# Performance work log

Hardware: AMD Instinct MI355X
Metric: run time of the kernel (lower is better)

The kernel has to match this reference:

```python
import jax, jax.numpy as jnp
import numpy as np

SCOPE = 2
N = 20
D = 64
CAP = 32
IN_CH = 64
OUT_CH = 64
FIN_CH = 64
WIDTH = 2 * SCOPE + 1


def setup_inputs() -> dict:
    key = jax.random.key(0)
    ks = jax.random.split(key, 7)
    dm = 3 * CAP + D  # memory feature dim: 3 relpos blocks + spatial embedding

    def w(k, fan_in, shape):
        return jax.random.normal(k, shape, jnp.float32) / np.sqrt(fan_in)

    return dict(
        spatial_embeddings=jax.random.normal(ks[0], (N, N, N, D), jnp.float32),
        relpos_w=jax.random.normal(ks[1], (WIDTH, CAP), jnp.float32) / np.sqrt(WIDTH * CAP),
        Wq=w(ks[2], D, (D, IN_CH)), bq=jnp.zeros((IN_CH,), jnp.float32),
        Wk=w(ks[3], dm, (dm, IN_CH)), bk=jnp.zeros((IN_CH,), jnp.float32),
        Wv=w(ks[4], dm, (dm, OUT_CH)), bv=jnp.zeros((OUT_CH,), jnp.float32),
        Wo=w(ks[5], OUT_CH, (OUT_CH, FIN_CH)), bo=jnp.zeros((FIN_CH,), jnp.float32),
    )


def reference(spatial_embeddings, relpos_w, Wq, bq, Wk, bk, Wv, bv, Wo, bo):
    n = spatial_embeddings.shape[0]
    w = WIDTH
    m = n + 2 * SCOPE  # padded grid size
    cap = relpos_w.shape[-1]

    # within_edges=False: zero-pad all three spatial axes by SCOPE
    se = jnp.pad(spatial_embeddings, ((SCOPE, SCOPE),) * 3 + ((0, 0),))
    central = SCOPE + jnp.arange(n)               # padded centre indices [n]
    off = jnp.arange(-SCOPE, SCOPE + 1)           # [w]
    idx = central[:, None] + off[None, :]         # [n, w] padded neighbour indices

    # relative-position cube: relpos_cube[x,y,z] = concat(r[x], r[y], r[z])
    r0 = jnp.broadcast_to(relpos_w[:, None, None, :], (w, w, w, cap))
    r1 = jnp.broadcast_to(relpos_w[None, :, None, :], (w, w, w, cap))
    r2 = jnp.broadcast_to(relpos_w[None, None, :, :], (w, w, w, cap))
    relpos_flat = jnp.concatenate([r0, r1, r2], axis=-1).reshape(w * w * w, 3 * cap)

    # neighbour gather replicating jnp.meshgrid(...)'s default 'xy' indexing:
    # cube[b, a, c] = se[ni[a], nj[b], nk[c]]
    ii = idx[:, None, None, None, :, None]        # (qi, a)
    jj = idx[None, :, None, :, None, None]        # (qj, b)
    kk = idx[None, None, :, None, None, :]        # (qk, c)
    nb = se[ii, jj, kk]                           # [n,n,n,w,w,w,D]
    nb = nb.reshape(n, n, n, w * w * w, -1)       # [n,n,n,w^3,D]

    # keys/values over memory = concat(relpos, neighbours); split the weight
    Wk_rel, Wk_nb = Wk[:3 * cap], Wk[3 * cap:]
    Wv_rel, Wv_nb = Wv[:3 * cap], Wv[3 * cap:]
    k_rel = relpos_flat @ Wk_rel + bk             # [w^3, IN_CH] (query-independent)
    v_rel = relpos_flat @ Wv_rel + bv             # [w^3, OUT_CH]
    keys = k_rel + jnp.einsum('xyzpd,dc->xyzpc', nb, Wk_nb)
    values = v_rel + jnp.einsum('xyzpd,dc->xyzpc', nb, Wv_nb)

    # centre embedding at padded index `central` == original unpadded embedding
    q = spatial_embeddings @ Wq + bq              # [n,n,n,IN_CH]
    logits = jnp.einsum('xyzc,xyzpc->xyzp', q, keys)

    # edge mask, built in (a,b,c) cube order (faithful to original's flatten order)
    valid = ((idx > SCOPE) & (idx < m - SCOPE)).astype(logits.dtype)  # [n, w]
    mask = (valid[:, None, None, :, None, None]
            * valid[None, :, None, None, :, None]
            * valid[None, None, :, None, None, :]).reshape(n, n, n, w * w * w)
    logits = logits - (1.0 - mask) * 1e9

    scores = jax.nn.softmax(logits, axis=-1)
    reweighted = jnp.einsum('xyzp,xyzpc->xyzc', scores, values)
    return reweighted @ Wo + bo                   # [n,n,n,FIN_CH]
```

## Files before the change

kernel.cpp:

```cpp
#include <hip/hip_runtime.h>

#define NN 20
#define NP 125
#define NV (NN*NN*NN)

__global__ __launch_bounds__(64) void prep(
        const float* __restrict__ rpw,
        const float* __restrict__ Wk, const float* __restrict__ bk,
        const float* __restrict__ Wv, const float* __restrict__ bv,
        const float* __restrict__ Wo,
        float* __restrict__ k_rel, float* __restrict__ vrelW,
        float* __restrict__ Wvo) {
    const int c = threadIdx.x;
    if (blockIdx.x < NP) {
        const int p = blockIdx.x;
        const int d3 = p / 25, d4 = (p / 5) % 5, d5 = p % 5;
        __shared__ float vtmp[64];
        float ak = bk[c], av = bv[c];
#pragma unroll
        for (int t = 0; t < 96; ++t) {
            const int blk = t >> 5, off = t & 31;
            const int row = (blk == 0) ? d3 : (blk == 1) ? d4 : d5;
            const float r = rpw[row * 32 + off];
            ak = fmaf(r, Wk[t * 64 + c], ak);
            av = fmaf(r, Wv[t * 64 + c], av);
        }
        k_rel[p * 64 + c] = ak;
        vtmp[c] = av;
        __syncthreads();
        float o = 0.f;
#pragma unroll 8
        for (int e = 0; e < 64; ++e)
            o = fmaf(vtmp[e], Wo[e * 64 + c], o);
        vrelW[p * 64 + c] = o;
    } else {
        const int d = blockIdx.x - NP;
        float acc = 0.f;
#pragma unroll 8
        for (int e = 0; e < 64; ++e)
            acc = fmaf(Wv[(96 + d) * 64 + e], Wo[e * 64 + c], acc);
        Wvo[d * 64 + c] = acc;
    }
}

__global__ __launch_bounds__(256) void qkv2(
        const float* __restrict__ SE,
        const float* __restrict__ Wq, const float* __restrict__ bq,
        const float* __restrict__ Wk, const float* __restrict__ Wvo,
        float* __restrict__ Q, float* __restrict__ Km, float* __restrict__ VW) {
    __shared__ float se_s[32][65];
    const int t = threadIdx.x;
    const int vbase = blockIdx.x * 32;
    {
        const float4* __restrict__ src = (const float4*)(SE + vbase * 64);
        const float4 a = src[t];
        const float4 b = src[t + 256];
        const int r0 = t >> 4,        c0 = (t & 15) * 4;
        const int r1 = (t + 256) >> 4;
        se_s[r0][c0 + 0] = a.x; se_s[r0][c0 + 1] = a.y;
        se_s[r0][c0 + 2] = a.z; se_s[r0][c0 + 3] = a.w;
        se_s[r1][c0 + 0] = b.x; se_s[r1][c0 + 1] = b.y;
        se_s[r1][c0 + 2] = b.z; se_s[r1][c0 + 3] = b.w;
    }
    __syncthreads();
    const int lane = t & 63, w = t >> 6;
    float aq[8], ak[8], av[8];
#pragma unroll
    for (int j = 0; j < 8; ++j) { aq[j] = bq[lane]; ak[j] = 0.f; av[j] = 0.f; }
#pragma unroll 8
    for (int d = 0; d < 64; ++d) {
        const float wq = Wq[d * 64 + lane];
        const float wk = Wk[(96 + d) * 64 + lane];
        const float wv = Wvo[d * 64 + lane];
#pragma unroll
        for (int j = 0; j < 8; ++j) {
            const float s = se_s[w * 8 + j][d];
            aq[j] = fmaf(s, wq, aq[j]);
            ak[j] = fmaf(s, wk, ak[j]);
            av[j] = fmaf(s, wv, av[j]);
        }
    }
#pragma unroll
    for (int j = 0; j < 8; ++j) {
        const int v = vbase + w * 8 + j;
        Q[v * 64 + lane]  = aq[j];
        Km[v * 64 + lane] = ak[j];
        VW[v * 64 + lane] = av[j];
    }
}

__global__ __launch_bounds__(512, 4) void attn4(
        const float* __restrict__ Q, const float* __restrict__ Km,
        const float* __restrict__ VW,
        const float* __restrict__ k_rel, const float* __restrict__ vrelW,
        const float* __restrict__ bo,
        float* __restrict__ out) {
    __shared__ float u[216 * 65];
    __shared__ float sc_s[8][128];

    const int tid  = threadIdx.x;
    const int lane = tid & 63;
    const int w    = tid >> 6;

    const int chunk = blockIdx.x & 7;
    const int idx   = blockIdx.x >> 3;
    const int cx = chunk >> 2, cy = (chunk >> 1) & 1, cz = chunk & 1;
    const int TX = cx * 5 + idx / 25;
    const int TY = cy * 5 + (idx / 5) % 5;
    const int TZ = cz * 5 + idx % 5;

    const int wx = w >> 2, wy = (w >> 1) & 1, wz = w & 1;
    const int x = TX * 2 + wx, y = TY * 2 + wy, z = TZ * 2 + wz;
    const int v = (x * NN + y) * NN + z;

    for (int i = tid; i < 216 * 16; i += 512) {
        const int row = i >> 4, ch = i & 15;
        const int ux = row / 36, uy = (row / 6) % 6, uz = row % 6;
        const int gX = TX * 2 - 2 + ux;
        const int gY = TY * 2 - 2 + uy;
        const int gZ = TZ * 2 - 2 + uz;
        float4 val = make_float4(0.f, 0.f, 0.f, 0.f);
        if ((unsigned)gX <= 19u && (unsigned)gY <= 19u && (unsigned)gZ <= 19u)
            val = ((const float4*)Km)[((gX * NN + gY) * NN + gZ) * 16 + ch];
        const int b = row * 65 + ch * 4;
        u[b] = val.x; u[b + 1] = val.y; u[b + 2] = val.z; u[b + 3] = val.w;
    }

    const float q = Q[v * 64 + lane];
    const int p0 = lane;
    const int p1 = lane + 64;
    const int p1c = (p1 < NP) ? p1 : (NP - 1);

    int e3 = p0 / 25, e4 = (p0 / 5) % 5, e5 = p0 % 5;
    const int row0 = 36 * (wx + e4) + 6 * (wy + e3) + (wz + e5);
    const bool mv0 = ((unsigned)(x + e3 - 3) <= 18u) &&
                     ((unsigned)(y + e4 - 3) <= 18u) &&
                     ((unsigned)(z + e5 - 3) <= 18u);
    e3 = p1c / 25; e4 = (p1c / 5) % 5; e5 = p1c % 5;
    const int row1 = 36 * (wx + e4) + 6 * (wy + e3) + (wz + e5);
    const bool mv1 = (p1 < NP) &&
                     ((unsigned)(x + e3 - 3) <= 18u) &&
                     ((unsigned)(y + e4 - 3) <= 18u) &&
                     ((unsigned)(z + e5 - 3) <= 18u);

    const float4* __restrict__ kr0 = (const float4*)(k_rel + p0 * 64);
    const float4* __restrict__ kr1 = (const float4*)(k_rel + p1c * 64);

    __syncthreads();

    float a0 = 0.f, a1 = 0.f;
#pragma unroll
    for (int i = 0; i < 16; ++i) {
        const float qa = __shfl(q, 4 * i + 0);
        const float qb = __shfl(q, 4 * i + 1);
        const float qc = __shfl(q, 4 * i + 2);
        const float qd = __shfl(q, 4 * i + 3);
        const float4 r0 = kr0[i], r1 = kr1[i];
        const int b0 = row0 * 65 + 4 * i;
        const int b1 = row1 * 65 + 4 * i;
        a0 = fmaf(u[b0] + r0.x, qa, a0);
        a0 = fmaf(u[b0 + 1] + r0.y, qb, a0);
        a0 = fmaf(u[b0 + 2] + r0.z, qc, a0);
        a0 = fmaf(u[b0 + 3] + r0.w, qd, a0);
        a1 = fmaf(u[b1] + r1.x, qa, a1);
        a1 = fmaf(u[b1 + 1] + r1.y, qb, a1);
        a1 = fmaf(u[b1 + 2] + r1.z, qc, a1);
        a1 = fmaf(u[b1 + 3] + r1.w, qd, a1);
    }
    const float l0 = mv0 ? a0 : -1e9f;
    const float l1 = mv1 ? a1 : -1e9f;

    float m = fmaxf(l0, l1);
#pragma unroll
    for (int d = 1; d < 64; d <<= 1) m = fmaxf(m, __shfl_xor(m, d));
    const float e0 = __expf(l0 - m);
    const float e1 = __expf(l1 - m);
    float ssum = e0 + e1;
#pragma unroll
    for (int d = 1; d < 64; d <<= 1) ssum += __shfl_xor(ssum, d);
    const float inv = 1.f / ssum;
    sc_s[w][p0] = e0 * inv;
    sc_s[w][p1] = e1 * inv;
    __syncthreads();

    for (int i = tid; i < 216 * 16; i += 512) {
        const int row = i >> 4, ch = i & 15;
        const int ux = row / 36, uy = (row / 6) % 6, uz = row % 6;
        const int gX = TX * 2 - 2 + ux;
        const int gY = TY * 2 - 2 + uy;
        const int gZ = TZ * 2 - 2 + uz;
        float4 val = make_float4(0.f, 0.f, 0.f, 0.f);
        if ((unsigned)gX <= 19u && (unsigned)gY <= 19u && (unsigned)gZ <= 19u)
            val = ((const float4*)VW)[((gX * NN + gY) * NN + gZ) * 16 + ch];
        const int b = row * 65 + ch * 4;
        u[b] = val.x; u[b + 1] = val.y; u[b + 2] = val.z; u[b + 3] = val.w;
    }
    __syncthreads();

    float A0 = 0.f, A1 = 0.f, A2 = 0.f, A3 = 0.f, A4 = 0.f;
    const float* __restrict__ vr = vrelW + lane;
#pragma unroll 5
    for (int g = 0; g < 25; ++g) {
        const int ge3 = g / 5, ge4 = g % 5;
        const int rb = 36 * (wx + ge4) + 6 * (wy + ge3) + wz;
        const int pb = g * 5;
        A0 = fmaf(sc_s[w][pb + 0], u[(rb + 0) * 65 + lane] + vr[(pb + 0) * 64], A0);
        A1 = fmaf(sc_s[w][pb + 1], u[(rb + 1) * 65 + lane] + vr[(pb + 1) * 64], A1);
        A2 = fmaf(sc_s[w][pb + 2], u[(rb + 2) * 65 + lane] + vr[(pb + 2) * 64], A2);
        A3 = fmaf(sc_s[w][pb + 3], u[(rb + 3) * 65 + lane] + vr[(pb + 3) * 64], A3);
        A4 = fmaf(sc_s[w][pb + 4], u[(rb + 4) * 65 + lane] + vr[(pb + 4) * 64], A4);
    }
    const float rw = ((A0 + A1) + (A2 + A3)) + A4;
    out[v * 64 + lane] = rw + bo[lane];
}

extern "C" void kernel_launch(void* const* d_in, const int* in_sizes, int n_in,
                              void* d_out, int out_size, void* d_ws, size_t ws_size,
                              hipStream_t stream) {
    const float* SE  = (const float*)d_in[0];
    const float* rpw = (const float*)d_in[1];
    const float* Wq  = (const float*)d_in[2];
    const float* bq  = (const float*)d_in[3];
    const float* Wk  = (const float*)d_in[4];
    const float* bk  = (const float*)d_in[5];
    const float* Wv  = (const float*)d_in[6];
    const float* bv  = (const float*)d_in[7];
    const float* Wo  = (const float*)d_in[8];
    const float* bo  = (const float*)d_in[9];
    float* out = (float*)d_out;

    float* ws    = (float*)d_ws;
    float* Q     = ws;
    float* Km    = ws + 512000;
    float* VW    = ws + 1024000;
    float* k_rel = ws + 1536000;
    float* vrelW = ws + 1544000;
    float* Wvo   = ws + 1552000;

    prep<<<NP + 64, 64, 0, stream>>>(rpw, Wk, bk, Wv, bv, Wo, k_rel, vrelW, Wvo);
    qkv2<<<NV / 32, 256, 0, stream>>>(SE, Wq, bq, Wk, Wvo, Q, Km, VW);
    attn4<<<1000, 512, 0, stream>>>(Q, Km, VW, k_rel, vrelW, bo, out);
}
```

Before: 134.9 us.

## Precompute q·k_rel in projection kernel, swizzle LDS, prefetch values into registers

The query-times-relative-key dot products are moved out of the attention kernel: the projection kernel now computes q·k_rel for all 125 offsets per voxel and writes them to a new workspace buffer. The attention kernel reads these and no longer adds k_rel inside its inner loop. Shared memory switches from a 65-float padded stride to a 68-float stride with XOR swizzle, so float4 LDS reads are possible. The VW halo is loaded into registers before the logits loop, overlapping global latency with compute, and shuffles become readlane. In exchange the projection kernel does more work, adds 4 MB of extra traffic and uses more registers.

```diff
diff --git a/kernel.cpp b/kernel.cpp
--- a/kernel.cpp
+++ b/kernel.cpp
@@ -3,6 +3,10 @@
 #define NN 20
 #define NP 125
 #define NV (NN*NN*NN)
+
+__device__ __forceinline__ float rlf(float v, int l) {
+    return __uint_as_float(__builtin_amdgcn_readlane(__float_as_uint(v), l));
+}
 
 __global__ __launch_bounds__(64) void prep(
         const float* __restrict__ rpw,
@@ -43,12 +47,15 @@
     }
 }
 
-__global__ __launch_bounds__(256) void qkv2(
+__global__ __launch_bounds__(256) void qkv4(
         const float* __restrict__ SE,
         const float* __restrict__ Wq, const float* __restrict__ bq,
         const float* __restrict__ Wk, const float* __restrict__ Wvo,
-        float* __restrict__ Q, float* __restrict__ Km, float* __restrict__ VW) {
+        const float* __restrict__ k_rel,
+        float* __restrict__ Q, float* __restrict__ Km, float* __restrict__ VW,
+        float* __restrict__ qkr) {
     __shared__ float se_s[32][65];
+    __shared__ __align__(16) float krs[125 * 68];
     const int t = threadIdx.x;
     const int vbase = blockIdx.x * 32;
     {
@@ -62,6 +69,12 @@
         se_s[r1][c0 + 0] = b.x; se_s[r1][c0 + 1] = b.y;
         se_s[r1][c0 + 2] = b.z; se_s[r1][c0 + 3] = b.w;
     }
+    for (int i = t; i < 125 * 16; i += 256) {
+        const int row = i >> 4, ch4 = (i & 15) * 4;
+        const float4 val = ((const float4*)k_rel)[row * 16 + (ch4 >> 2)];
+        const int xk = ((row >> 3) & 7) << 2;
+        *(float4*)&krs[row * 68 + (ch4 ^ xk)] = val;
+    }
     __syncthreads();
     const int lane = t & 63, w = t >> 6;
     float aq[8], ak[8], av[8];
@@ -87,15 +100,40 @@
         Km[v * 64 + lane] = ak[j];
         VW[v * 64 + lane] = av[j];
     }
-}
-
-__global__ __launch_bounds__(512, 4) void attn4(
+    const int p0 = lane;
+    const int p1c = (lane + 64 < NP) ? (lane + 64) : (NP - 1);
+    const int xk0 = ((p0 >> 3) & 7) << 2;
+    const int xk1 = ((p1c >> 3) & 7) << 2;
+#pragma unroll
+    for (int j = 0; j < 8; ++j) {
+        float d0 = 0.f, d1 = 0.f;
+#pragma unroll
+        for (int i = 0; i < 16; ++i) {
+            const float qa = rlf(aq[j], 4 * i + 0);
+            const float qb = rlf(aq[j], 4 * i + 1);
+            const float qc = rlf(aq[j], 4 * i + 2);
+            const float qd = rlf(aq[j], 4 * i + 3);
+            const float4 k0 = *(const float4*)&krs[p0 * 68 + ((4 * i) ^ xk0)];
+            const float4 k1 = *(const float4*)&krs[p1c * 68 + ((4 * i) ^ xk1)];
+            d0 = fmaf(k0.x, qa, d0); d0 = fmaf(k0.y, qb, d0);
+            d0 = fmaf(k0.z, qc, d0); d0 = fmaf(k0.w, qd, d0);
+            d1 = fmaf(k1.x, qa, d1); d1 = fmaf(k1.y, qb, d1);
+            d1 = fmaf(k1.z, qc, d1); d1 = fmaf(k1.w, qd, d1);
+        }
+        const int v = vbase + w * 8 + j;
+        qkr[v * 128 + lane] = d0;
+        qkr[v * 128 + 64 + lane] = d1;
+    }
+}
+
+#define XU(row) ((((row >> 3) ^ (row >> 6)) & 7) << 2)
+
+__global__ __launch_bounds__(512, 4) void attn9(
         const float* __restrict__ Q, const float* __restrict__ Km,
-        const float* __restrict__ VW,
-        const float* __restrict__ k_rel, const float* __restrict__ vrelW,
-        const float* __restrict__ bo,
+        const float* __restrict__ VW, const float* __restrict__ qkr,
+        const float* __restrict__ vrelW, const float* __restrict__ bo,
         float* __restrict__ out) {
-    __shared__ float u[216 * 65];
+    __shared__ __align__(16) float u[216 * 68];
     __shared__ float sc_s[8][128];
 
     const int tid  = threadIdx.x;
@@ -114,19 +152,21 @@
     const int v = (x * NN + y) * NN + z;
 
     for (int i = tid; i < 216 * 16; i += 512) {
-        const int row = i >> 4, ch = i & 15;
+        const int row = i >> 4, ch4 = (i & 15) * 4;
         const int ux = row / 36, uy = (row / 6) % 6, uz = row % 6;
         const int gX = TX * 2 - 2 + ux;
         const int gY = TY * 2 - 2 + uy;
         const int gZ = TZ * 2 - 2 + uz;
         float4 val = make_float4(0.f, 0.f, 0.f, 0.f);
         if ((unsigned)gX <= 19u && (unsigned)gY <= 19u && (unsigned)gZ <= 19u)
-            val = ((const float4*)Km)[((gX * NN + gY) * NN + gZ) * 16 + ch];
-        const int b = row * 65 + ch * 4;
-        u[b] = val.x; u[b + 1] = val.y; u[b + 2] = val.z; u[b + 3] = val.w;
+            val = ((const float4*)Km)[((gX * NN + gY) * NN + gZ) * 16 + (ch4 >> 2)];
+        *(float4*)&u[row * 68 + (ch4 ^ XU(row))] = val;
     }
 
     const float q = Q[v * 64 + lane];
+    const float qk0 = qkr[v * 128 + lane];
+    const float qk1 = qkr[v * 128 + 64 + lane];
+
     const int p0 = lane;
     const int p1 = lane + 64;
     const int p1c = (p1 < NP) ? p1 : (NP - 1);
@@ -142,33 +182,43 @@
                      ((unsigned)(x + e3 - 3) <= 18u) &&
                      ((unsigned)(y + e4 - 3) <= 18u) &&
                      ((unsigned)(z + e5 - 3) <= 18u);
-
-    const float4* __restrict__ kr0 = (const float4*)(k_rel + p0 * 64);
-    const float4* __restrict__ kr1 = (const float4*)(k_rel + p1c * 64);
-
-    __syncthreads();
+    const int xu0 = XU(row0), xu1 = XU(row1);
+
+    __syncthreads();
+
+    float4 vwreg[7];
+#pragma unroll
+    for (int k = 0; k < 7; ++k) {
+        const int i = tid + 512 * k;
+        float4 val = make_float4(0.f, 0.f, 0.f, 0.f);
+        if (i < 216 * 16) {
+            const int row = i >> 4, ch = i & 15;
+            const int ux = row / 36, uy = (row / 6) % 6, uz = row % 6;
+            const int gX = TX * 2 - 2 + ux;
+            const int gY = TY * 2 - 2 + uy;
+            const int gZ = TZ * 2 - 2 + uz;
+            if ((unsigned)gX <= 19u && (unsigned)gY <= 19u && (unsigned)gZ <= 19u)
+                val = ((const float4*)VW)[((gX * NN + gY) * NN + gZ) * 16 + ch];
+        }
+        vwreg[k] = val;
+    }
 
     float a0 = 0.f, a1 = 0.f;
 #pragma unroll
     for (int i = 0; i < 16; ++i) {
-        const float qa = __shfl(q, 4 * i + 0);
-        const float qb = __shfl(q, 4 * i + 1);
-        const float qc = __shfl(q, 4 * i + 2);
-        const float qd = __shfl(q, 4 * i + 3);
-        const float4 r0 = kr0[i], r1 = kr1[i];
-        const int b0 = row0 * 65 + 4 * i;
-        const int b1 = row1 * 65 + 4 * i;
-        a0 = fmaf(u[b0] + r0.x, qa, a0);
-        a0 = fmaf(u[b0 + 1] + r0.y, qb, a0);
-        a0 = fmaf(u[b0 + 2] + r0.z, qc, a0);
-        a0 = fmaf(u[b0 + 3] + r0.w, qd, a0);
-        a1 = fmaf(u[b1] + r1.x, qa, a1);
-        a1 = fmaf(u[b1 + 1] + r1.y, qb, a1);
-        a1 = fmaf(u[b1 + 2] + r1.z, qc, a1);
-        a1 = fmaf(u[b1 + 3] + r1.w, qd, a1);
-    }
-    const float l0 = mv0 ? a0 : -1e9f;
-    const float l1 = mv1 ? a1 : -1e9f;
+        const float qa = rlf(q, 4 * i + 0);
+        const float qb = rlf(q, 4 * i + 1);
+        const float qc = rlf(q, 4 * i + 2);
+        const float qd = rlf(q, 4 * i + 3);
+        const float4 k0 = *(const float4*)&u[row0 * 68 + ((4 * i) ^ xu0)];
+        const float4 k1 = *(const float4*)&u[row1 * 68 + ((4 * i) ^ xu1)];
+        a0 = fmaf(k0.x, qa, a0); a0 = fmaf(k0.y, qb, a0);
+        a0 = fmaf(k0.z, qc, a0); a0 = fmaf(k0.w, qd, a0);
+        a1 = fmaf(k1.x, qa, a1); a1 = fmaf(k1.y, qb, a1);
+        a1 = fmaf(k1.z, qc, a1); a1 = fmaf(k1.w, qd, a1);
+    }
+    const float l0 = mv0 ? a0 + qk0 : -1e9f;
+    const float l1 = mv1 ? a1 + qk1 : -1e9f;
 
     float m = fmaxf(l0, l1);
 #pragma unroll
@@ -183,17 +233,13 @@
     sc_s[w][p1] = e1 * inv;
     __syncthreads();
 
-    for (int i = tid; i < 216 * 16; i += 512) {
-        const int row = i >> 4, ch = i & 15;
-        const int ux = row / 36, uy = (row / 6) % 6, uz = row % 6;
-        const int gX = TX * 2 - 2 + ux;
-        const int gY = TY * 2 - 2 + uy;
-        const int gZ = TZ * 2 - 2 + uz;
-        float4 val = make_float4(0.f, 0.f, 0.f, 0.f);
-        if ((unsigned)gX <= 19u && (unsigned)gY <= 19u && (unsigned)gZ <= 19u)
-            val = ((const float4*)VW)[((gX * NN + gY) * NN + gZ) * 16 + ch];
-        const int b = row * 65 + ch * 4;
-        u[b] = val.x; u[b + 1] = val.y; u[b + 2] = val.z; u[b + 3] = val.w;
+#pragma unroll
+    for (int k = 0; k < 7; ++k) {
+        const int i = tid + 512 * k;
+        if (i < 216 * 16) {
+            const int row = i >> 4, ch4 = (i & 15) * 4;
+            *(float4*)&u[row * 68 + (ch4 ^ XU(row))] = vwreg[k];
+        }
     }
     __syncthreads();
 
@@ -204,11 +250,15 @@
         const int ge3 = g / 5, ge4 = g % 5;
         const int rb = 36 * (wx + ge4) + 6 * (wy + ge3) + wz;
         const int pb = g * 5;
-        A0 = fmaf(sc_s[w][pb + 0], u[(rb + 0) * 65 + lane] + vr[(pb + 0) * 64], A0);
-        A1 = fmaf(sc_s[w][pb + 1], u[(rb + 1) * 65 + lane] + vr[(pb + 1) * 64], A1);
-        A2 = fmaf(sc_s[w][pb + 2], u[(rb + 2) * 65 + lane] + vr[(pb + 2) * 64], A2);
-        A3 = fmaf(sc_s[w][pb + 3], u[(rb + 3) * 65 + lane] + vr[(pb + 3) * 64], A3);
-        A4 = fmaf(sc_s[w][pb + 4], u[(rb + 4) * 65 + lane] + vr[(pb + 4) * 64], A4);
+#define STEP(J, ACC)                                                           \
+        {                                                                      \
+            const int rr = rb + (J);                                           \
+            const float sc = sc_s[w][pb + (J)];                                \
+            ACC = fmaf(sc, u[rr * 68 + (lane ^ XU(rr))] + vr[(pb + (J)) * 64], \
+                       ACC);                                                   \
+        }
+        STEP(0, A0) STEP(1, A1) STEP(2, A2) STEP(3, A3) STEP(4, A4)
+#undef STEP
     }
     const float rw = ((A0 + A1) + (A2 + A3)) + A4;
     out[v * 64 + lane] = rw + bo[lane];
@@ -236,8 +286,9 @@
     float* k_rel = ws + 1536000;
     float* vrelW = ws + 1544000;
     float* Wvo   = ws + 1552000;
+    float* qkr   = ws + 1556096;
 
     prep<<<NP + 64, 64, 0, stream>>>(rpw, Wk, bk, Wv, bv, Wo, k_rel, vrelW, Wvo);
-    qkv2<<<NV / 32, 256, 0, stream>>>(SE, Wq, bq, Wk, Wvo, Q, Km, VW);
-    attn4<<<1000, 512, 0, stream>>>(Q, Km, VW, k_rel, vrelW, bo, out);
-}
+    qkv4<<<NV / 32, 256, 0, stream>>>(SE, Wq, bq, Wk, Wvo, k_rel, Q, Km, VW, qkr);
+    attn9<<<1000, 512, 0, stream>>>(Q, Km, VW, qkr, vrelW, bo, out);
+}
```

Result: slower. 144.8 us (+7.4%).
